# Kernel tuning notes

Measured on AMD Instinct MI355X. Metric: run time of the kernel, lower is better.

The kernel has to match this reference:

```python
import jax, jax.numpy as jnp
import numpy as np

NN_SIZE = 10  # k nearest neighbors (includes the point itself)
EPS = 1e-8


def batch_normals(points_nchw, nn_size):
    # points_nchw: (B, 3, N)
    x = jnp.transpose(points_nchw, (0, 2, 1))  # (B, N, 3)
    sq = jnp.sum(x * x, axis=-1)  # (B, N)
    # pairwise squared distances (B, N, N)
    d2 = sq[:, :, None] + sq[:, None, :] - 2.0 * jnp.einsum('bnd,bmd->bnm', x, x)
    _, idx = jax.lax.top_k(-d2, nn_size)  # (B, N, k) nearest-neighbor indices
    # irregular gather of neighborhoods: (B, N, k, 3)
    neigh = jax.vmap(lambda p, i: p[i])(x, idx)
    centered = neigh - jnp.mean(neigh, axis=2, keepdims=True)
    # local 3x3 covariance per point
    cov = jnp.einsum('bnki,bnkj->bnij', centered, centered) / nn_size
    _, vecs = jnp.linalg.eigh(cov)  # eigenvalues ascending
    normals = vecs[..., 0]  # eigenvector of smallest eigenvalue, (B, N, 3), unit norm
    return jnp.transpose(normals, (0, 2, 1))  # (B, 3, N)


def setup_inputs() -> dict:
    key = jax.random.key(0)
    k1, k2 = jax.random.split(key)
    pred = jax.random.normal(k1, (8, 3, 4096), dtype=jnp.float32)
    gt = jax.random.normal(k2, (8, 3, 4096), dtype=jnp.float32)
    return {"pred": pred, "gt": gt}


def reference(pred, gt):
    pn = batch_normals(pred, NN_SIZE)  # (B, 3, N)
    gn = batch_normals(gt, NN_SIZE)    # (B, 3, N)
    # cosine similarity along the channel (coordinate) dim
    dot = jnp.sum(pn * gn, axis=1)
    denom = jnp.sqrt(jnp.sum(pn * pn, axis=1)) * jnp.sqrt(jnp.sum(gn * gn, axis=1))
    cos = dot / jnp.maximum(denom, EPS)
    return jnp.mean(1.0 - jnp.abs(cos))
```

## Files before the change

kernel.cpp:

```cpp
#include <hip/hip_runtime.h>
#include <float.h>
#include <math.h>

#define BATCH 8
#define NPTS 4096
#define KNN 10
#define BN (BATCH * NPTS)
#define TPB 1024
#define WAVES 16
#define QPB 128
#define SEGC (NPTS / WAVES)
#define GRIDX (NPTS / QPB)
#define KB_STRIDE (2 * KNN + 1)

__device__ inline float med3f(float x, float a, float b) {
    return __builtin_amdgcn_fmed3f(x, a, b);
}

#define INSERT(karr, key)                                              \
    do {                                                               \
        _Pragma("unroll")                                              \
        for (int _j = KNN - 1; _j >= 1; --_j)                          \
            karr[_j] = med3f((key), karr[_j - 1], karr[_j]);           \
        karr[0] = fminf((key), karr[0]);                               \
    } while (0)

#define PROC(_p, _gi, ka, kb)                                          \
    do {                                                               \
        float _d0 = fmaf((_p).z, a0z, fmaf((_p).y, a0y, fmaf((_p).x, a0x, (_p).w))); \
        float _d1 = fmaf((_p).z, a1z, fmaf((_p).y, a1y, fmaf((_p).x, a1x, (_p).w))); \
        float _k0 = __uint_as_float((__float_as_uint(_d0) & 0xFFFFF000u) | (_gi)); \
        float _k1 = __uint_as_float((__float_as_uint(_d1) & 0xFFFFF000u) | (_gi)); \
        INSERT(ka, _k0);                                               \
        INSERT(kb, _k1);                                               \
    } while (0)

#define PROC8(P, _gi, ka, kb)                                          \
    do {                                                               \
        PROC(P##0, (_gi) + 0, ka, kb);                                 \
        PROC(P##1, (_gi) + 1, ka, kb);                                 \
        PROC(P##2, (_gi) + 2, ka, kb);                                 \
        PROC(P##3, (_gi) + 3, ka, kb);                                 \
        PROC(P##4, (_gi) + 4, ka, kb);                                 \
        PROC(P##5, (_gi) + 5, ka, kb);                                 \
        PROC(P##6, (_gi) + 6, ka, kb);                                 \
        PROC(P##7, (_gi) + 7, ka, kb);                                 \
    } while (0)

#define LOAD8(P, _off)                                                 \
    do {                                                               \
        P##0 = pts[(_off) + 0]; P##1 = pts[(_off) + 1];                \
        P##2 = pts[(_off) + 2]; P##3 = pts[(_off) + 3];                \
        P##4 = pts[(_off) + 4]; P##5 = pts[(_off) + 5];                \
        P##6 = pts[(_off) + 6]; P##7 = pts[(_off) + 7];                \
    } while (0)

__device__ inline void smallest_eigvec(float a00, float a01, float a02,
                                       float a11, float a12, float a22,
                                       float& vx, float& vy, float& vz) {
    float p1 = a01 * a01 + a02 * a02 + a12 * a12;
    float q = (a00 + a11 + a22) * (1.0f / 3.0f);
    float b00 = a00 - q, b11 = a11 - q, b22 = a22 - q;
    float p2 = b00 * b00 + b11 * b11 + b22 * b22 + 2.0f * p1;
    float p = sqrtf(p2 * (1.0f / 6.0f));
    if (p < 1e-20f) { vx = 1.0f; vy = 0.0f; vz = 0.0f; return; }
    float ip = 1.0f / p;
    float c00 = b00 * ip, c01 = a01 * ip, c02 = a02 * ip;
    float c11 = b11 * ip, c12 = a12 * ip, c22 = b22 * ip;
    float detB = c00 * (c11 * c22 - c12 * c12)
               - c01 * (c01 * c22 - c12 * c02)
               + c02 * (c01 * c12 - c11 * c02);
    float r = 0.5f * detB;
    r = fminf(1.0f, fmaxf(-1.0f, r));
    float phi = acosf(r) * (1.0f / 3.0f);
    float lmin = q + 2.0f * p * cosf(phi + 2.0943951023931953f);

    float m00 = a00 - lmin, m11 = a11 - lmin, m22 = a22 - lmin;
    float r0x = m00, r0y = a01, r0z = a02;
    float r1x = a01, r1y = m11, r1z = a12;
    float r2x = a02, r2y = a12, r2z = m22;
    float c0x = r0y * r1z - r0z * r1y, c0y = r0z * r1x - r0x * r1z, c0z = r0x * r1y - r0y * r1x;
    float c1x = r0y * r2z - r0z * r2y, c1y = r0z * r2x - r0x * r2z, c1z = r0x * r2y - r0y * r2x;
    float c2x = r1y * r2z - r1z * r2y, c2y = r1z * r2x - r1x * r2z, c2z = r1x * r2y - r1y * r2x;
    float n0 = c0x * c0x + c0y * c0y + c0z * c0z;
    float n1 = c1x * c1x + c1y * c1y + c1z * c1z;
    float n2 = c2x * c2x + c2y * c2y + c2z * c2z;
    float bx = c0x, by = c0y, bz = c0z, bnm = n0;
    if (n1 > bnm) { bx = c1x; by = c1y; bz = c1z; bnm = n1; }
    if (n2 > bnm) { bx = c2x; by = c2y; bz = c2z; bnm = n2; }
    if (bnm < 1e-30f) { vx = 1.0f; vy = 0.0f; vz = 0.0f; return; }
    float inv = rsqrtf(bnm);
    vx = bx * inv; vy = by * inv; vz = bz * inv;
}

#define SCAN_CLOUD(basep, ka, kb)                                      \
    do {                                                               \
        _Pragma("unroll")                                              \
        for (int _j = 0; _j < KNN; ++_j) { ka[_j] = FLT_MAX; kb[_j] = FLT_MAX; } \
        const float a0x = -2.0f * (basep)[pt0];                        \
        const float a0y = -2.0f * (basep)[NPTS + pt0];                 \
        const float a0z = -2.0f * (basep)[2 * NPTS + pt0];             \
        const float a1x = -2.0f * (basep)[pt1];                        \
        const float a1y = -2.0f * (basep)[NPTS + pt1];                 \
        const float a1z = -2.0f * (basep)[2 * NPTS + pt1];             \
        for (int _i = tid; _i < NPTS; _i += TPB) {                     \
            float _x = (basep)[_i];                                    \
            float _y = (basep)[NPTS + _i];                             \
            float _z = (basep)[2 * NPTS + _i];                         \
            pts[_i] = make_float4(_x, _y, _z, fmaf(_x, _x, fmaf(_y, _y, _z * _z))); \
        }                                                              \
        __syncthreads();                                               \
        {                                                              \
            const unsigned _gb = (unsigned)s0;                         \
            float4 A0, A1, A2, A3, A4, A5, A6, A7;                     \
            float4 B0, B1, B2, B3, B4, B5, B6, B7;                     \
            LOAD8(A, s0);                                              \
            __builtin_amdgcn_sched_barrier(0);                         \
            for (int _c = 0; _c < SEGC; _c += 16) {                    \
                LOAD8(B, s0 + _c + 8);                                 \
                __builtin_amdgcn_sched_barrier(0);                     \
                PROC8(A, _gb + (unsigned)_c, ka, kb);                  \
                __builtin_amdgcn_sched_barrier(0);                     \
                LOAD8(A, s0 + _c + 16);       \
                __builtin_amdgcn_sched_barrier(0);                     \
                PROC8(B, _gb + (unsigned)_c + 8u, ka, kb);             \
                __builtin_amdgcn_sched_barrier(0);                     \
            }                                                          \
        }                                                              \
        __syncthreads();         \
             \
        for (int _half = WAVES / 2; _half >= 1; _half >>= 1) {         \
            if (w >= _half && w < 2 * _half) {                         \
                float* _dst = keybuf + ((w - _half) * 64 + lane) * KB_STRIDE; \
                _Pragma("unroll")                                      \
                for (int _j = 0; _j < KNN; ++_j) { _dst[_j] = ka[_j]; _dst[KNN + _j] = kb[_j]; } \
            }                                                          \
            __syncthreads();                                           \
            if (w < _half) {                                           \
                const float* _src = keybuf + (w * 64 + lane) * KB_STRIDE; \
                _Pragma("unroll")                                      \
                for (int _j = 0; _j < KNN; ++_j) {                     \
                    float _sa = _src[_j], _sb = _src[KNN + _j];        \
                    INSERT(ka, _sa);                                   \
                    INSERT(kb, _sb);                                   \
                }                                                      \
            }                                                          \
            __syncthreads();                                           \
        }                                                              \
    } while (0)

#define COMPUTE_NORMAL(karr, basep, vx, vy, vz)                        \
    do {                                                               \
        float _sx = 0.f, _sy = 0.f, _sz = 0.f;                         \
        float _sxx = 0.f, _sxy = 0.f, _sxz = 0.f;                      \
        float _syy = 0.f, _syz = 0.f, _szz = 0.f;                      \
        _Pragma("unroll")                                              \
        for (int _j = 0; _j < KNN; ++_j) {                             \
            int _idx = (int)(__float_as_uint(karr[_j]) & 0xFFFu);      \
            float _x = (basep)[_idx];                                  \
            float _y = (basep)[NPTS + _idx];                           \
            float _z = (basep)[2 * NPTS + _idx];                       \
            _sx += _x; _sy += _y; _sz += _z;                           \
            _sxx = fmaf(_x, _x, _sxx); _sxy = fmaf(_x, _y, _sxy); _sxz = fmaf(_x, _z, _sxz); \
            _syy = fmaf(_y, _y, _syy); _syz = fmaf(_y, _z, _syz); _szz = fmaf(_z, _z, _szz); \
        }                                                              \
        const float _iK = 1.0f / KNN;                                  \
        float _mx = _sx * _iK, _my = _sy * _iK, _mz = _sz * _iK;       \
        smallest_eigvec(_sxx * _iK - _mx * _mx, _sxy * _iK - _mx * _my, \
                        _sxz * _iK - _mx * _mz, _syy * _iK - _my * _my, \
                        _syz * _iK - _my * _mz, _szz * _iK - _mz * _mz, \
                        vx, vy, vz);                                   \
    } while (0)

__global__ void zero_out_kernel(float* __restrict__ out) {
    if (threadIdx.x == 0) out[0] = 0.0f;
}

__global__ __launch_bounds__(TPB, 4) void knn_normal_loss(
    const float* __restrict__ pred, const float* __restrict__ gt,
    float* __restrict__ out) {
    __shared__ float4 pts[NPTS + 8];

    const int b = blockIdx.y;
    const float* __restrict__ baseP = pred + b * 3 * NPTS;
    const float* __restrict__ baseG = gt + b * 3 * NPTS;
    const int tid = threadIdx.x;
    const int lane = tid & 63;
    const int w = tid >> 6;
    const int s0 = w * SEGC;
    float* keybuf = (float*)pts;

    const int pt0 = blockIdx.x * QPB + lane;
    const int pt1 = pt0 + 64;

    float kP0[KNN], kP1[KNN];
    float kG0[KNN], kG1[KNN];

    SCAN_CLOUD(baseP, kP0, kP1);
    SCAN_CLOUD(baseG, kG0, kG1);

    if (w == 0) {
        float acc;
        {
            float pvx, pvy, pvz, gvx, gvy, gvz;
            COMPUTE_NORMAL(kP0, baseP, pvx, pvy, pvz);
            COMPUTE_NORMAL(kG0, baseG, gvx, gvy, gvz);
            float dot = pvx * gvx + pvy * gvy + pvz * gvz;
            float npn = sqrtf(pvx * pvx + pvy * pvy + pvz * pvz);
            float ngn = sqrtf(gvx * gvx + gvy * gvy + gvz * gvz);
            acc = 1.0f - fabsf(dot / fmaxf(npn * ngn, 1e-8f));
        }
        {
            float pvx, pvy, pvz, gvx, gvy, gvz;
            COMPUTE_NORMAL(kP1, baseP, pvx, pvy, pvz);
            COMPUTE_NORMAL(kG1, baseG, gvx, gvy, gvz);
            float dot = pvx * gvx + pvy * gvy + pvz * gvz;
            float npn = sqrtf(pvx * pvx + pvy * pvy + pvz * pvz);
            float ngn = sqrtf(gvx * gvx + gvy * gvy + gvz * gvz);
            acc += 1.0f - fabsf(dot / fmaxf(npn * ngn, 1e-8f));
        }
        for (int off = 32; off > 0; off >>= 1) acc += __shfl_down(acc, off);
        if (lane == 0) atomicAdd(out, acc * (1.0f / (float)BN));
    }
}

extern "C" void kernel_launch(void* const* d_in, const int* in_sizes, int n_in,
                              void* d_out, int out_size, void* d_ws, size_t ws_size,
                              hipStream_t stream) {
    const float* pred = (const float*)d_in[0];
    const float* gt = (const float*)d_in[1];
    float* out = (float*)d_out;

    zero_out_kernel<<<1, 64, 0, stream>>>(out);
    dim3 grid(GRIDX, BATCH);
    knn_normal_loss<<<grid, TPB, 0, stream>>>(pred, gt, out);
}
```

Before: 171.3 us.

## Split clouds across grid z, process four queries per lane, separate loss kernel

Each block now handles a single cloud (pred or gt, chosen by grid z) and 256 query points, with every lane tracking four queries instead of two. Each shared-memory point load is therefore reused across four distance/insert computations, and each block reloads only one cloud instead of two. Normals are computed in parallel by four waves reading neighbours from shared memory instead of global memory, stored to a global buffer, and reduced by a new cosine-loss kernel. In exchange each lane holds twice as many top-k registers (possible occupancy loss), keybuf gets its own shared allocation, and there is one more kernel launch.

Result: no change. 172.6 us (+0.7%).

```diff
diff --git a/kernel.cpp b/kernel.cpp
--- a/kernel.cpp
+++ b/kernel.cpp
@@ -8,10 +8,12 @@
 #define BN (BATCH * NPTS)
 #define TPB 1024
 #define WAVES 16
-#define QPB 128
+#define Q 4
+#define QPB (64 * Q)
 #define SEGC (NPTS / WAVES)
-#define GRIDX (NPTS / QPB)
-#define KB_STRIDE (2 * KNN + 1)
+#define KB_STRIDE (Q * KNN + 1)
+
+__device__ float4 g_nrm[2 * BN];
 
 __device__ inline float med3f(float x, float a, float b) {
     return __builtin_amdgcn_fmed3f(x, a, b);
@@ -25,34 +27,34 @@
         karr[0] = fminf((key), karr[0]);                               \
     } while (0)
 
-#define PROC(_p, _gi, ka, kb)                                          \
+#define PROC(_p, _gi)                                                  \
     do {                                                               \
         float _d0 = fmaf((_p).z, a0z, fmaf((_p).y, a0y, fmaf((_p).x, a0x, (_p).w))); \
         float _d1 = fmaf((_p).z, a1z, fmaf((_p).y, a1y, fmaf((_p).x, a1x, (_p).w))); \
+        float _d2 = fmaf((_p).z, a2z, fmaf((_p).y, a2y, fmaf((_p).x, a2x, (_p).w))); \
+        float _d3 = fmaf((_p).z, a3z, fmaf((_p).y, a3y, fmaf((_p).x, a3x, (_p).w))); \
         float _k0 = __uint_as_float((__float_as_uint(_d0) & 0xFFFFF000u) | (_gi)); \
         float _k1 = __uint_as_float((__float_as_uint(_d1) & 0xFFFFF000u) | (_gi)); \
-        INSERT(ka, _k0);                                               \
-        INSERT(kb, _k1);                                               \
-    } while (0)
-
-#define PROC8(P, _gi, ka, kb)                                          \
-    do {                                                               \
-        PROC(P##0, (_gi) + 0, ka, kb);                                 \
-        PROC(P##1, (_gi) + 1, ka, kb);                                 \
-        PROC(P##2, (_gi) + 2, ka, kb);                                 \
-        PROC(P##3, (_gi) + 3, ka, kb);                                 \
-        PROC(P##4, (_gi) + 4, ka, kb);                                 \
-        PROC(P##5, (_gi) + 5, ka, kb);                                 \
-        PROC(P##6, (_gi) + 6, ka, kb);                                 \
-        PROC(P##7, (_gi) + 7, ka, kb);                                 \
-    } while (0)
-
-#define LOAD8(P, _off)                                                 \
+        float _k2 = __uint_as_float((__float_as_uint(_d2) & 0xFFFFF000u) | (_gi)); \
+        float _k3 = __uint_as_float((__float_as_uint(_d3) & 0xFFFFF000u) | (_gi)); \
+        INSERT(kq0, _k0);                                              \
+        INSERT(kq1, _k1);                                              \
+        INSERT(kq2, _k2);                                              \
+        INSERT(kq3, _k3);                                              \
+    } while (0)
+
+#define PROC4(P, _gi)                                                  \
+    do {                                                               \
+        PROC(P##0, (_gi) + 0);                                         \
+        PROC(P##1, (_gi) + 1);                                         \
+        PROC(P##2, (_gi) + 2);                                         \
+        PROC(P##3, (_gi) + 3);                                         \
+    } while (0)
+
+#define LOAD4(P, _off)                                                 \
     do {                                                               \
         P##0 = pts[(_off) + 0]; P##1 = pts[(_off) + 1];                \
         P##2 = pts[(_off) + 2]; P##3 = pts[(_off) + 3];                \
-        P##4 = pts[(_off) + 4]; P##5 = pts[(_off) + 5];                \
-        P##6 = pts[(_off) + 6]; P##7 = pts[(_off) + 7];                \
     } while (0)
 
 __device__ inline void smallest_eigvec(float a00, float a01, float a02,
@@ -93,135 +95,131 @@
     vx = bx * inv; vy = by * inv; vz = bz * inv;
 }
 
-#define SCAN_CLOUD(basep, ka, kb)                                      \
-    do {                                                               \
-        _Pragma("unroll")                                              \
-        for (int _j = 0; _j < KNN; ++_j) { ka[_j] = FLT_MAX; kb[_j] = FLT_MAX; } \
-        const float a0x = -2.0f * (basep)[pt0];                        \
-        const float a0y = -2.0f * (basep)[NPTS + pt0];                 \
-        const float a0z = -2.0f * (basep)[2 * NPTS + pt0];             \
-        const float a1x = -2.0f * (basep)[pt1];                        \
-        const float a1y = -2.0f * (basep)[NPTS + pt1];                 \
-        const float a1z = -2.0f * (basep)[2 * NPTS + pt1];             \
-        for (int _i = tid; _i < NPTS; _i += TPB) {                     \
-            float _x = (basep)[_i];                                    \
-            float _y = (basep)[NPTS + _i];                             \
-            float _z = (basep)[2 * NPTS + _i];                         \
-            pts[_i] = make_float4(_x, _y, _z, fmaf(_x, _x, fmaf(_y, _y, _z * _z))); \
-        }                                                              \
-        __syncthreads();                                               \
-        {                                                              \
-            const unsigned _gb = (unsigned)s0;                         \
-            float4 A0, A1, A2, A3, A4, A5, A6, A7;                     \
-            float4 B0, B1, B2, B3, B4, B5, B6, B7;                     \
-            LOAD8(A, s0);                                              \
-            __builtin_amdgcn_sched_barrier(0);                         \
-            for (int _c = 0; _c < SEGC; _c += 16) {                    \
-                LOAD8(B, s0 + _c + 8);                                 \
-                __builtin_amdgcn_sched_barrier(0);                     \
-                PROC8(A, _gb + (unsigned)_c, ka, kb);                  \
-                __builtin_amdgcn_sched_barrier(0);                     \
-                LOAD8(A, s0 + _c + 16);       \
-                __builtin_amdgcn_sched_barrier(0);                     \
-                PROC8(B, _gb + (unsigned)_c + 8u, ka, kb);             \
-                __builtin_amdgcn_sched_barrier(0);                     \
-            }                                                          \
-        }                                                              \
-        __syncthreads();         \
-             \
-        for (int _half = WAVES / 2; _half >= 1; _half >>= 1) {         \
-            if (w >= _half && w < 2 * _half) {                         \
-                float* _dst = keybuf + ((w - _half) * 64 + lane) * KB_STRIDE; \
-                _Pragma("unroll")                                      \
-                for (int _j = 0; _j < KNN; ++_j) { _dst[_j] = ka[_j]; _dst[KNN + _j] = kb[_j]; } \
-            }                                                          \
-            __syncthreads();                                           \
-            if (w < _half) {                                           \
-                const float* _src = keybuf + (w * 64 + lane) * KB_STRIDE; \
-                _Pragma("unroll")                                      \
-                for (int _j = 0; _j < KNN; ++_j) {                     \
-                    float _sa = _src[_j], _sb = _src[KNN + _j];        \
-                    INSERT(ka, _sa);                                   \
-                    INSERT(kb, _sb);                                   \
-                }                                                      \
-            }                                                          \
-            __syncthreads();                                           \
-        }                                                              \
-    } while (0)
-
-#define COMPUTE_NORMAL(karr, basep, vx, vy, vz)                        \
-    do {                                                               \
-        float _sx = 0.f, _sy = 0.f, _sz = 0.f;                         \
-        float _sxx = 0.f, _sxy = 0.f, _sxz = 0.f;                      \
-        float _syy = 0.f, _syz = 0.f, _szz = 0.f;                      \
-        _Pragma("unroll")                                              \
-        for (int _j = 0; _j < KNN; ++_j) {                             \
-            int _idx = (int)(__float_as_uint(karr[_j]) & 0xFFFu);      \
-            float _x = (basep)[_idx];                                  \
-            float _y = (basep)[NPTS + _idx];                           \
-            float _z = (basep)[2 * NPTS + _idx];                       \
-            _sx += _x; _sy += _y; _sz += _z;                           \
-            _sxx = fmaf(_x, _x, _sxx); _sxy = fmaf(_x, _y, _sxy); _sxz = fmaf(_x, _z, _sxz); \
-            _syy = fmaf(_y, _y, _syy); _syz = fmaf(_y, _z, _syz); _szz = fmaf(_z, _z, _szz); \
-        }                                                              \
-        const float _iK = 1.0f / KNN;                                  \
-        float _mx = _sx * _iK, _my = _sy * _iK, _mz = _sz * _iK;       \
-        smallest_eigvec(_sxx * _iK - _mx * _mx, _sxy * _iK - _mx * _my, \
-                        _sxz * _iK - _mx * _mz, _syy * _iK - _my * _my, \
-                        _syz * _iK - _my * _mz, _szz * _iK - _mz * _mz, \
-                        vx, vy, vz);                                   \
-    } while (0)
-
 __global__ void zero_out_kernel(float* __restrict__ out) {
     if (threadIdx.x == 0) out[0] = 0.0f;
 }
 
-__global__ __launch_bounds__(TPB, 4) void knn_normal_loss(
-    const float* __restrict__ pred, const float* __restrict__ gt,
-    float* __restrict__ out) {
+__global__ __launch_bounds__(TPB, 4) void knn_normals(
+    const float* __restrict__ pred, const float* __restrict__ gt) {
     __shared__ float4 pts[NPTS + 8];
+    __shared__ float keybuf[8 * 64 * KB_STRIDE];
 
     const int b = blockIdx.y;
-    const float* __restrict__ baseP = pred + b * 3 * NPTS;
-    const float* __restrict__ baseG = gt + b * 3 * NPTS;
+    const int cloud = blockIdx.z;
+    const float* __restrict__ base = (cloud ? gt : pred) + b * 3 * NPTS;
     const int tid = threadIdx.x;
     const int lane = tid & 63;
     const int w = tid >> 6;
     const int s0 = w * SEGC;
-    float* keybuf = (float*)pts;
-
-    const int pt0 = blockIdx.x * QPB + lane;
-    const int pt1 = pt0 + 64;
-
-    float kP0[KNN], kP1[KNN];
-    float kG0[KNN], kG1[KNN];
-
-    SCAN_CLOUD(baseP, kP0, kP1);
-    SCAN_CLOUD(baseG, kG0, kG1);
+    const int qbase = blockIdx.x * QPB;
+
+    for (int i = tid; i < NPTS; i += TPB) {
+        float x = base[i];
+        float y = base[NPTS + i];
+        float z = base[2 * NPTS + i];
+        pts[i] = make_float4(x, y, z, fmaf(x, x, fmaf(y, y, z * z)));
+    }
+    __syncthreads();
+
+    const int q0 = qbase + lane;
+    const float a0x = -2.0f * pts[q0].x,       a0y = -2.0f * pts[q0].y,       a0z = -2.0f * pts[q0].z;
+    const float a1x = -2.0f * pts[q0 + 64].x,  a1y = -2.0f * pts[q0 + 64].y,  a1z = -2.0f * pts[q0 + 64].z;
+    const float a2x = -2.0f * pts[q0 + 128].x, a2y = -2.0f * pts[q0 + 128].y, a2z = -2.0f * pts[q0 + 128].z;
+    const float a3x = -2.0f * pts[q0 + 192].x, a3y = -2.0f * pts[q0 + 192].y, a3z = -2.0f * pts[q0 + 192].z;
+
+    float kq0[KNN], kq1[KNN], kq2[KNN], kq3[KNN];
+#pragma unroll
+    for (int j = 0; j < KNN; ++j) { kq0[j] = FLT_MAX; kq1[j] = FLT_MAX; kq2[j] = FLT_MAX; kq3[j] = FLT_MAX; }
+
+    {
+        const unsigned gb = (unsigned)s0;
+        float4 A0, A1, A2, A3;
+        float4 B0, B1, B2, B3;
+        LOAD4(A, s0);
+        __builtin_amdgcn_sched_barrier(0);
+        for (int c = 0; c < SEGC; c += 8) {
+            LOAD4(B, s0 + c + 4);
+            __builtin_amdgcn_sched_barrier(0);
+            PROC4(A, gb + (unsigned)c);
+            __builtin_amdgcn_sched_barrier(0);
+            LOAD4(A, s0 + c + 8);
+            __builtin_amdgcn_sched_barrier(0);
+            PROC4(B, gb + (unsigned)c + 4u);
+            __builtin_amdgcn_sched_barrier(0);
+        }
+    }
+
+    for (int half = WAVES / 2; half >= 1; half >>= 1) {
+        if (w >= half && w < 2 * half) {
+            float* dst = keybuf + ((w - half) * 64 + lane) * KB_STRIDE;
+#pragma unroll
+            for (int j = 0; j < KNN; ++j) {
+                dst[j] = kq0[j];
+                dst[KNN + j] = kq1[j];
+                dst[2 * KNN + j] = kq2[j];
+                dst[3 * KNN + j] = kq3[j];
+            }
+        }
+        __syncthreads();
+        if (w < half) {
+            const float* src = keybuf + (w * 64 + lane) * KB_STRIDE;
+#pragma unroll
+            for (int j = 0; j < KNN; ++j) {
+                float s0v = src[j], s1v = src[KNN + j], s2v = src[2 * KNN + j], s3v = src[3 * KNN + j];
+                INSERT(kq0, s0v);
+                INSERT(kq1, s1v);
+                INSERT(kq2, s2v);
+                INSERT(kq3, s3v);
+            }
+        }
+        __syncthreads();
+    }
 
     if (w == 0) {
-        float acc;
-        {
-            float pvx, pvy, pvz, gvx, gvy, gvz;
-            COMPUTE_NORMAL(kP0, baseP, pvx, pvy, pvz);
-            COMPUTE_NORMAL(kG0, baseG, gvx, gvy, gvz);
-            float dot = pvx * gvx + pvy * gvy + pvz * gvz;
-            float npn = sqrtf(pvx * pvx + pvy * pvy + pvz * pvz);
-            float ngn = sqrtf(gvx * gvx + gvy * gvy + gvz * gvz);
-            acc = 1.0f - fabsf(dot / fmaxf(npn * ngn, 1e-8f));
-        }
-        {
-            float pvx, pvy, pvz, gvx, gvy, gvz;
-            COMPUTE_NORMAL(kP1, baseP, pvx, pvy, pvz);
-            COMPUTE_NORMAL(kG1, baseG, gvx, gvy, gvz);
-            float dot = pvx * gvx + pvy * gvy + pvz * gvz;
-            float npn = sqrtf(pvx * pvx + pvy * pvy + pvz * pvz);
-            float ngn = sqrtf(gvx * gvx + gvy * gvy + gvz * gvz);
-            acc += 1.0f - fabsf(dot / fmaxf(npn * ngn, 1e-8f));
-        }
-        for (int off = 32; off > 0; off >>= 1) acc += __shfl_down(acc, off);
-        if (lane == 0) atomicAdd(out, acc * (1.0f / (float)BN));
-    }
+        float* dst = keybuf + lane * KB_STRIDE;
+#pragma unroll
+        for (int j = 0; j < KNN; ++j) {
+            dst[j] = kq0[j];
+            dst[KNN + j] = kq1[j];
+            dst[2 * KNN + j] = kq2[j];
+            dst[3 * KNN + j] = kq3[j];
+        }
+    }
+    __syncthreads();
+    if (w < Q) {
+        const float* src = keybuf + lane * KB_STRIDE + w * KNN;
+        float sx = 0.f, sy = 0.f, sz = 0.f;
+        float sxx = 0.f, sxy = 0.f, sxz = 0.f;
+        float syy = 0.f, syz = 0.f, szz = 0.f;
+#pragma unroll
+        for (int j = 0; j < KNN; ++j) {
+            int idx = (int)(__float_as_uint(src[j]) & 0xFFFu);
+            float4 nb = pts[idx];
+            sx += nb.x; sy += nb.y; sz += nb.z;
+            sxx = fmaf(nb.x, nb.x, sxx); sxy = fmaf(nb.x, nb.y, sxy); sxz = fmaf(nb.x, nb.z, sxz);
+            syy = fmaf(nb.y, nb.y, syy); syz = fmaf(nb.y, nb.z, syz); szz = fmaf(nb.z, nb.z, szz);
+        }
+        const float iK = 1.0f / KNN;
+        float mx = sx * iK, my = sy * iK, mz = sz * iK;
+        float vx, vy, vz;
+        smallest_eigvec(sxx * iK - mx * mx, sxy * iK - mx * my,
+                        sxz * iK - mx * mz, syy * iK - my * my,
+                        syz * iK - my * mz, szz * iK - mz * mz,
+                        vx, vy, vz);
+        g_nrm[(cloud * BATCH + b) * NPTS + qbase + w * 64 + lane] = make_float4(vx, vy, vz, 0.f);
+    }
+}
+
+__global__ __launch_bounds__(256) void cos_loss_kernel(float* __restrict__ out) {
+    const int i = blockIdx.x * 256 + threadIdx.x;
+    float4 p = g_nrm[i];
+    float4 g = g_nrm[BN + i];
+    float dot = p.x * g.x + p.y * g.y + p.z * g.z;
+    float npn = sqrtf(p.x * p.x + p.y * p.y + p.z * p.z);
+    float ngn = sqrtf(g.x * g.x + g.y * g.y + g.z * g.z);
+    float acc = 1.0f - fabsf(dot / fmaxf(npn * ngn, 1e-8f));
+    for (int off = 32; off > 0; off >>= 1) acc += __shfl_down(acc, off);
+    if ((threadIdx.x & 63) == 0) atomicAdd(out, acc * (1.0f / (float)BN));
 }
 
 extern "C" void kernel_launch(void* const* d_in, const int* in_sizes, int n_in,
@@ -232,6 +230,7 @@
     float* out = (float*)d_out;
 
     zero_out_kernel<<<1, 64, 0, stream>>>(out);
-    dim3 grid(GRIDX, BATCH);
-    knn_normal_loss<<<grid, TPB, 0, stream>>>(pred, gt, out);
-}
+    dim3 grid(NPTS / QPB, BATCH, 2);
+    knn_normals<<<grid, TPB, 0, stream>>>(pred, gt);
+    cos_loss_kernel<<<dim3(BN / 256), 256, 0, stream>>>(out);
+}
```
